# Optimization experiments

Measured on AMD Instinct MI355X. Metric: run time of the kernel, lower is better.

## Reference

```python
import jax, jax.numpy as jnp
import numpy as np


def setup_inputs() -> dict:
    key = jax.random.key(0)
    ks = jax.random.split(key, 7)
    B, S, D, KP = 16, 4096, 64, 256  # batch*heads, seq_len, head_dim, linformer proj dim
    Q = jax.random.normal(ks[0], (B, S, D), dtype=jnp.float32)
    K = jax.random.normal(ks[1], (B, S, D), dtype=jnp.float32)
    V = jax.random.normal(ks[2], (B, S, D), dtype=jnp.float32)
    E_w = jax.random.normal(ks[3], (KP, S), dtype=jnp.float32) / np.sqrt(S)
    E_b = jax.random.normal(ks[4], (KP,), dtype=jnp.float32) * 0.01
    F_w = jax.random.normal(ks[5], (KP, S), dtype=jnp.float32) / np.sqrt(S)
    F_b = jax.random.normal(ks[6], (KP,), dtype=jnp.float32) * 0.01
    return {"Q": Q, "K": K, "V": V, "E_w": E_w, "E_b": E_b, "F_w": F_w, "F_b": F_b}


def reference(Q, K, V, E_w, E_b, F_w, F_b):
    # Linformer head (mask=None path); dropout is identity at inference.
    dim_k = K.shape[-1]
    scale = 1.0 / jnp.sqrt(jnp.float32(dim_k))
    # K.permute(0,2,1) -> [B, d, S]; E projects seq axis S -> k: [B, d, k]
    Kp = jnp.einsum('bsd,ks->bdk', K, E_w) + E_b  # [B, d, k]
    # V.permute -> F -> permute back: [B, k, d]
    Vp = jnp.einsum('bsd,ks->bkd', V, F_w) + F_b[None, :, None]  # [B, k, d]
    scores = jnp.einsum('bsd,bdk->bsk', Q, Kp) * scale  # [B, S, k]
    attn = jax.nn.softmax(scores, axis=-1)
    out = jnp.einsum('bsk,bkd->bsd', attn, Vp)  # [B, S, d]
    return (out, attn)
```

## Files before the change

kernel.cpp:

```cpp
#include <hip/hip_runtime.h>


#define B_  16
#define S_  4096
#define D_  64
#define KP_ 256

typedef short v8s __attribute__((ext_vector_type(8)));
typedef float v4f __attribute__((ext_vector_type(4)));

__device__ __forceinline__ short f2bf(float x) {
    union { float f; unsigned u; } v; v.f = x;
    unsigned r = v.u + 0x7FFFu + ((v.u >> 16) & 1u);
    return (short)(r >> 16);
}
__device__ __forceinline__ float bf2f(short h) {
    union { float f; unsigned u; } v; v.u = ((unsigned)(unsigned short)h) << 16;
    return v.f;
}

__global__ __launch_bounds__(256)
void wcvt_kernel(const float* __restrict__ E_w, const float* __restrict__ F_w,
                 short* __restrict__ Whi, short* __restrict__ Wlo)
{
    const int p = blockIdx.y;
    const float* W = p ? F_w : E_w;
    const size_t i4 = (size_t)blockIdx.x * 256 + threadIdx.x;
    float4 v = ((const float4*)W)[i4];
    short4 h, lo;
    h.x = f2bf(v.x); lo.x = f2bf(v.x - bf2f(h.x));
    h.y = f2bf(v.y); lo.y = f2bf(v.y - bf2f(h.y));
    h.z = f2bf(v.z); lo.z = f2bf(v.z - bf2f(h.z));
    h.w = f2bf(v.w); lo.w = f2bf(v.w - bf2f(h.w));
    const int k  = (int)(i4 >> 10);
    const int s0 = (int)(i4 & 1023) << 2;
    const size_t fo = (((size_t)p * 16 + (k >> 4)) * 128 + (s0 >> 5)) * 512
                    + (size_t)(((k & 15) + ((s0 >> 3) & 3) * 16) * 8) + (s0 & 7);
    *(short4*)(Whi + fo) = h;
    *(short4*)(Wlo + fo) = lo;
}

__global__ __launch_bounds__(512, 4)
void proj_mfma_kernel(const float* __restrict__ Kg, const float* __restrict__ Vg,
                      const short* __restrict__ Whi, const short* __restrict__ Wlo,
                      float* __restrict__ PpartK, float* __restrict__ PpartV)
{
    const int sc = blockIdx.x;
    const int p  = blockIdx.y;
    const int b  = blockIdx.z;

    const float* src = (p ? Vg : Kg) + ((size_t)b * S_ + sc * 256) * D_;

    __shared__ __align__(16) short Af[2][2][4][512];

    const int t  = threadIdx.x;
    const int wv = t >> 6;
    const int l  = t & 63;
    const int k16 = wv * 2;

    const size_t wbase = (((size_t)p * 16 + k16) * 128 + sc * 8) * 512 + (size_t)l * 8;

    v4f acc[2][4];
#pragma unroll
    for (int i = 0; i < 2; ++i)
#pragma unroll
        for (int m = 0; m < 4; ++m) acc[i][m] = (v4f){0.f, 0.f, 0.f, 0.f};

    const bool do_stage = (t < 256);
    const int sd   = t & 63;
    const int soct = (t >> 6) & 3;
    const int smt  = sd >> 4;
    const int sfl  = (sd & 15) + soct * 16;

    float g[8];
    if (do_stage) {
        const float* sp = src + (size_t)(soct * 8) * D_ + sd;
#pragma unroll
        for (int j = 0; j < 8; ++j) g[j] = sp[(size_t)j * D_];
        v8s hi, lo;
#pragma unroll
        for (int j = 0; j < 8; ++j) { short h = f2bf(g[j]); hi[j] = h; lo[j] = f2bf(g[j] - bf2f(h)); }
        *(v8s*)&Af[0][0][smt][sfl * 8] = hi;
        *(v8s*)&Af[0][1][smt][sfl * 8] = lo;
    }
    __syncthreads();

    for (int st = 0; st < 8; ++st) {
        const int cur = st & 1;
        if (st + 1 < 8 && do_stage) {
            const float* sp = src + (size_t)((st + 1) * 32 + soct * 8) * D_ + sd;
#pragma unroll
            for (int j = 0; j < 8; ++j) g[j] = sp[(size_t)j * D_];
        }
        v8s wh[2], wl2[2];
#pragma unroll
        for (int i = 0; i < 2; ++i) {
            size_t o = wbase + (size_t)i * 65536 + (size_t)st * 512;
            wh[i]  = *(const v8s*)(Whi + o);
            wl2[i] = *(const v8s*)(Wlo + o);
        }
        v8s sh[4], sl[4];
#pragma unroll
        for (int m = 0; m < 4; ++m) {
            sh[m] = *(const v8s*)&Af[cur][0][m][l * 8];
            sl[m] = *(const v8s*)&Af[cur][1][m][l * 8];
        }
        if (p == 0) {
#pragma unroll
            for (int i = 0; i < 2; ++i)
#pragma unroll
                for (int m = 0; m < 4; ++m) {
                    acc[i][m] = __builtin_amdgcn_mfma_f32_16x16x32_bf16(wh[i],  sh[m], acc[i][m], 0, 0, 0);
                    acc[i][m] = __builtin_amdgcn_mfma_f32_16x16x32_bf16(wh[i],  sl[m], acc[i][m], 0, 0, 0);
                    acc[i][m] = __builtin_amdgcn_mfma_f32_16x16x32_bf16(wl2[i], sh[m], acc[i][m], 0, 0, 0);
                }
        } else {
#pragma unroll
            for (int i = 0; i < 2; ++i)
#pragma unroll
                for (int m = 0; m < 4; ++m) {
                    acc[i][m] = __builtin_amdgcn_mfma_f32_16x16x32_bf16(sh[m], wh[i],  acc[i][m], 0, 0, 0);
                    acc[i][m] = __builtin_amdgcn_mfma_f32_16x16x32_bf16(sl[m], wh[i],  acc[i][m], 0, 0, 0);
                    acc[i][m] = __builtin_amdgcn_mfma_f32_16x16x32_bf16(sh[m], wl2[i], acc[i][m], 0, 0, 0);
                }
        }
        if (st + 1 < 8 && do_stage) {
            v8s hi, lo;
#pragma unroll
            for (int j = 0; j < 8; ++j) { short h = f2bf(g[j]); hi[j] = h; lo[j] = f2bf(g[j] - bf2f(h)); }
            *(v8s*)&Af[cur ^ 1][0][smt][sfl * 8] = hi;
            *(v8s*)&Af[cur ^ 1][1][smt][sfl * 8] = lo;
        }
        __syncthreads();
    }

    const int krow0 = wv * 32;
    if (p == 0) {
        float* outp = PpartK + ((size_t)sc * B_ + b) * (KP_ * D_);
#pragma unroll
        for (int i = 0; i < 2; ++i)
#pragma unroll
            for (int m = 0; m < 4; ++m)
#pragma unroll
                for (int r = 0; r < 4; ++r) {
                    int k = krow0 + i * 16 + (l >> 4) * 4 + r;
                    int d = m * 16 + (l & 15);
                    outp[(size_t)k * D_ + d] = acc[i][m][r];
                }
    } else {
        float* outp = PpartV + ((size_t)sc * B_ + b) * (KP_ * D_);
#pragma unroll
        for (int i = 0; i < 2; ++i)
#pragma unroll
            for (int m = 0; m < 4; ++m)
#pragma unroll
                for (int r = 0; r < 4; ++r) {
                    int d = m * 16 + (l >> 4) * 4 + r;
                    int k = krow0 + i * 16 + (l & 15);
                    outp[(size_t)d * KP_ + k] = acc[i][m][r];
                }
    }
}

__global__ __launch_bounds__(256)
void reduce_kernel(const float* __restrict__ PpartK, const float* __restrict__ PpartV,
                   const float* __restrict__ E_b, const float* __restrict__ F_b,
                   short* __restrict__ Kp_hi, short* __restrict__ Kp_lo,
                   short* __restrict__ Vp_hi)
{
    const int j    = blockIdx.x * 256 + threadIdx.x;
    const int side = j >> 16;
    const int i4   = j & 65535;
    const int flat = i4 * 4;
    const int b    = flat >> 14;
    const int dk   = flat & 16383;

    if (side == 0) {
        float4 a = make_float4(0.f, 0.f, 0.f, 0.f);
#pragma unroll
        for (int sc = 0; sc < 16; ++sc) {
            float4 v = *(const float4*)(PpartK + ((size_t)sc * B_ + b) * (KP_ * D_) + dk);
            a.x += v.x; a.y += v.y; a.z += v.z; a.w += v.w;
        }
        const int k = dk >> 6, d = dk & 63;
        float be = E_b[k];
        a.x += be; a.y += be; a.z += be; a.w += be;
        short4 h, lo;
        h.x = f2bf(a.x); lo.x = f2bf(a.x - bf2f(h.x));
        h.y = f2bf(a.y); lo.y = f2bf(a.y - bf2f(h.y));
        h.z = f2bf(a.z); lo.z = f2bf(a.z - bf2f(h.z));
        h.w = f2bf(a.w); lo.w = f2bf(a.w - bf2f(h.w));
        const size_t fo = (((size_t)b * 2 + (d >> 5)) * 16 + (k >> 4)) * 512
                        + (size_t)((k & 15) + ((d >> 3) & 3) * 16) * 8 + (d & 7);
        *(short4*)(Kp_hi + fo) = h;
        *(short4*)(Kp_lo + fo) = lo;
    } else {
        float4 a = make_float4(0.f, 0.f, 0.f, 0.f);
#pragma unroll
        for (int sc = 0; sc < 16; ++sc) {
            float4 v = *(const float4*)(PpartV + ((size_t)sc * B_ + b) * (KP_ * D_) + dk);
            a.x += v.x; a.y += v.y; a.z += v.z; a.w += v.w;
        }
        const int d = dk >> 8, k = dk & 255;
        float4 bf = *(const float4*)(F_b + k);
        a.x += bf.x; a.y += bf.y; a.z += bf.z; a.w += bf.w;
        short4 h;
        h.x = f2bf(a.x); h.y = f2bf(a.y); h.z = f2bf(a.z); h.w = f2bf(a.w);
        const size_t fo = (((size_t)b * 8 + (k >> 5)) * 4 + (d >> 4)) * 512
                        + (size_t)((d & 15) + ((k >> 3) & 3) * 16) * 8 + (k & 7);
        *(short4*)(Vp_hi + fo) = h;
    }
}

__global__ __launch_bounds__(256, 3)
void attn_mfma_kernel(const float* __restrict__ Qg,
                      const short* __restrict__ Kp_hi, const short* __restrict__ Kp_lo,
                      const short* __restrict__ Vp_hi,
                      float* __restrict__ attn_out, float* __restrict__ outg)
{
    const int st = blockIdx.x;
    const int b  = blockIdx.y;
    const int t  = threadIdx.x;
    const int wv = t >> 6;
    const int l  = t & 63;

    __shared__ __align__(16) short smem[64 * 264];
    __shared__ __align__(16) float Fst[4][4][264];
    short (*Qf)[2][4][512] = (short (*)[2][4][512])smem;
    short* Pl  = smem;
    short* KLl = smem + 8192;
    short* KLh = (short*)&Fst[0][0][0];

    {
        const int s    = t & 63;
        const int doct = t >> 6;
        const float* qrow = Qg + ((size_t)b * S_ + st * 64 + s) * D_;
        const int mt = s >> 4, fl = (s & 15) + doct * 16;
#pragma unroll
        for (int kd = 0; kd < 2; ++kd) {
            float4 v0 = *(const float4*)(qrow + kd * 32 + doct * 8);
            float4 v1 = *(const float4*)(qrow + kd * 32 + doct * 8 + 4);
            float gq[8] = {v0.x, v0.y, v0.z, v0.w, v1.x, v1.y, v1.z, v1.w};
            v8s hi, lo;
#pragma unroll
            for (int jj = 0; jj < 8; ++jj) { short h = f2bf(gq[jj]); hi[jj] = h; lo[jj] = f2bf(gq[jj] - bf2f(h)); }
            *(v8s*)&Qf[kd][0][mt][fl * 8] = hi;
            *(v8s*)&Qf[kd][1][mt][fl * 8] = lo;
        }
    }
    __syncthreads();

    v4f acc2[16];
#pragma unroll
    for (int nt = 0; nt < 16; ++nt) acc2[nt] = (v4f){0.f, 0.f, 0.f, 0.f};
#pragma unroll
    for (int kd = 0; kd < 2; ++kd) {
        {
            const size_t tbl = (((size_t)b * 2 + kd) * 16) * 512;
            const int4* gh = (const int4*)(Kp_hi + tbl);
            const int4* gl = (const int4*)(Kp_lo + tbl);
            int4* lh = (int4*)KLh;
            int4* ll = (int4*)KLl;
#pragma unroll
            for (int i = 0; i < 4; ++i) lh[t + i * 256] = gh[t + i * 256];
#pragma unroll
            for (int i = 0; i < 4; ++i) ll[t + i * 256] = gl[t + i * 256];
        }
        __syncthreads();
        v8s Ah = *(const v8s*)&Qf[kd][0][wv][l * 8];
        v8s Al = *(const v8s*)&Qf[kd][1][wv][l * 8];
#pragma unroll
        for (int nt = 0; nt < 16; ++nt) {
            v8s Bh = *(const v8s*)&KLh[nt * 512 + l * 8];
            v8s Bl = *(const v8s*)&KLl[nt * 512 + l * 8];
            acc2[nt] = __builtin_amdgcn_mfma_f32_16x16x32_bf16(Ah, Bh, acc2[nt], 0, 0, 0);
            acc2[nt] = __builtin_amdgcn_mfma_f32_16x16x32_bf16(Al, Bh, acc2[nt], 0, 0, 0);
            acc2[nt] = __builtin_amdgcn_mfma_f32_16x16x32_bf16(Ah, Bl, acc2[nt], 0, 0, 0);
        }
        __syncthreads();
    }

    int4 vstg[4];
    {
        const int4* gv = (const int4*)(Vp_hi + (size_t)b * 16384);
#pragma unroll
        for (int i = 0; i < 4; ++i) vstg[i] = gv[t + i * 256];
    }

    const float scale = 0.125f;
    float* attn_b = attn_out + ((size_t)b * S_ + st * 64) * KP_;
    const int g = l >> 4;
#pragma unroll
    for (int r = 0; r < 4; ++r) {
        float m = -3.4e38f;
#pragma unroll
        for (int nt = 0; nt < 16; ++nt) m = fmaxf(m, acc2[nt][r]);
        m = fmaxf(m, __shfl_xor(m, 1));
        m = fmaxf(m, __shfl_xor(m, 2));
        m = fmaxf(m, __shfl_xor(m, 4));
        m = fmaxf(m, __shfl_xor(m, 8));
        float sum = 0.f;
#pragma unroll
        for (int nt = 0; nt < 16; ++nt) {
            float e = __expf((acc2[nt][r] - m) * scale);
            acc2[nt][r] = e; sum += e;
        }
        sum += __shfl_xor(sum, 1);
        sum += __shfl_xor(sum, 2);
        sum += __shfl_xor(sum, 4);
        sum += __shfl_xor(sum, 8);
        const float inv = 1.f / sum;
        const int s_loc = wv * 16 + g * 4 + r;
#pragma unroll
        for (int nt = 0; nt < 16; ++nt) {
            float pv = acc2[nt][r] * inv;
            Fst[wv][g][nt * 16 + (l & 15)] = pv;
            Pl[s_loc * 264 + nt * 16 + (l & 15)] = f2bf(pv);
        }
#pragma unroll
        for (int gg = 0; gg < 4; ++gg) {
            float4 vv = *(const float4*)&Fst[wv][gg][l * 4];
            *(float4*)(attn_b + (size_t)(wv * 16 + gg * 4 + r) * KP_ + l * 4) = vv;
        }
    }
    __syncthreads();
    {
        int4* lv = (int4*)KLh;
#pragma unroll
        for (int i = 0; i < 4; ++i) lv[t + i * 256] = vstg[i];
    }
    {
        const int4* gv2 = (const int4*)(Vp_hi + (size_t)b * 16384 + 8192);
#pragma unroll
        for (int i = 0; i < 4; ++i) vstg[i] = gv2[t + i * 256];
    }
    __syncthreads();
    v4f acc3[4];
#pragma unroll
    for (int nt = 0; nt < 4; ++nt) acc3[nt] = (v4f){0.f, 0.f, 0.f, 0.f};
#pragma unroll
    for (int kc = 0; kc < 4; ++kc) {
        v8s A3 = *(const v8s*)&Pl[(wv * 16 + (l & 15)) * 264 + kc * 32 + (l >> 4) * 8];
#pragma unroll
        for (int nt = 0; nt < 4; ++nt) {
            v8s B3 = *(const v8s*)&KLh[(kc * 4 + nt) * 512 + l * 8];
            acc3[nt] = __builtin_amdgcn_mfma_f32_16x16x32_bf16(A3, B3, acc3[nt], 0, 0, 0);
        }
    }
    __syncthreads();
    {
        int4* lv = (int4*)KLh;
#pragma unroll
        for (int i = 0; i < 4; ++i) lv[t + i * 256] = vstg[i];
    }
    __syncthreads();
#pragma unroll
    for (int kc = 4; kc < 8; ++kc) {
        v8s A3 = *(const v8s*)&Pl[(wv * 16 + (l & 15)) * 264 + kc * 32 + (l >> 4) * 8];
#pragma unroll
        for (int nt = 0; nt < 4; ++nt) {
            v8s B3 = *(const v8s*)&KLh[((kc - 4) * 4 + nt) * 512 + l * 8];
            acc3[nt] = __builtin_amdgcn_mfma_f32_16x16x32_bf16(A3, B3, acc3[nt], 0, 0, 0);
        }
    }
    float* out_b = outg + ((size_t)b * S_ + st * 64) * D_;
#pragma unroll
    for (int nt = 0; nt < 4; ++nt)
#pragma unroll
        for (int r = 0; r < 4; ++r) {
            int s_loc = wv * 16 + (l >> 4) * 4 + r;
            out_b[(size_t)s_loc * D_ + nt * 16 + (l & 15)] = acc3[nt][r];
        }
}

extern "C" void kernel_launch(void* const* d_in, const int* in_sizes, int n_in,
                              void* d_out, int out_size, void* d_ws, size_t ws_size,
                              hipStream_t stream) {
    const float* Q   = (const float*)d_in[0];
    const float* K   = (const float*)d_in[1];
    const float* V   = (const float*)d_in[2];
    const float* E_w = (const float*)d_in[3];
    const float* E_b = (const float*)d_in[4];
    const float* F_w = (const float*)d_in[5];
    const float* F_b = (const float*)d_in[6];

    float* out  = (float*)d_out;
    float* attn = out + (size_t)B_ * S_ * D_;

    short* Whi   = (short*)d_ws;
    short* Wlo   = Whi + (size_t)2 * KP_ * S_;
    short* Kp_hi = Wlo + (size_t)2 * KP_ * S_;
    short* Kp_lo = Kp_hi + (size_t)B_ * KP_ * D_;
    short* Vp_hi = Kp_lo + (size_t)B_ * KP_ * D_;

    float* PpartK = attn;
    float* PpartV = attn + (size_t)16 * B_ * KP_ * D_;

    wcvt_kernel<<<dim3(KP_ * S_ / 4 / 256, 2), 256, 0, stream>>>(E_w, F_w, Whi, Wlo);
    proj_mfma_kernel<<<dim3(16, 2, B_), 512, 0, stream>>>(K, V, Whi, Wlo, PpartK, PpartV);
    reduce_kernel<<<dim3(512), 256, 0, stream>>>(PpartK, PpartV, E_b, F_b, Kp_hi, Kp_lo, Vp_hi);
    attn_mfma_kernel<<<dim3(S_ / 64, B_), 256, 0, stream>>>(Q, Kp_hi, Kp_lo, Vp_hi, attn, out);
}
```

Measured before the change: 189.6 us.

## Process two batches per projection block to reuse weight fragments

Each projection block now handles two batch entries, with all 512 threads staging K/V data (256 per batch) into a doubled shared buffer. The weight hi/lo fragments loaded from global memory are reused across both batches, which halves weight traffic and doubles MFMA work per load. The cost is double the accumulator registers, which is why launch bounds drop to 2 blocks per SM, and the grid is halved to 256 blocks, lowering parallelism.

```diff
diff --git a/kernel.cpp b/kernel.cpp
--- a/kernel.cpp
+++ b/kernel.cpp
@@ -40,18 +40,18 @@
     *(short4*)(Wlo + fo) = lo;
 }
 
-__global__ __launch_bounds__(512, 4)
+__global__ __launch_bounds__(512, 2)
 void proj_mfma_kernel(const float* __restrict__ Kg, const float* __restrict__ Vg,
                       const short* __restrict__ Whi, const short* __restrict__ Wlo,
                       float* __restrict__ PpartK, float* __restrict__ PpartV)
 {
     const int sc = blockIdx.x;
     const int p  = blockIdx.y;
-    const int b  = blockIdx.z;
-
-    const float* src = (p ? Vg : Kg) + ((size_t)b * S_ + sc * 256) * D_;
-
-    __shared__ __align__(16) short Af[2][2][4][512];
+    const int bp = blockIdx.z;
+
+    const float* srcB = (p ? Vg : Kg);
+
+    __shared__ __align__(16) short Af[2][2][2][4][512];
 
     const int t  = threadIdx.x;
     const int wv = t >> 6;
@@ -60,35 +60,39 @@
 
     const size_t wbase = (((size_t)p * 16 + k16) * 128 + sc * 8) * 512 + (size_t)l * 8;
 
-    v4f acc[2][4];
-#pragma unroll
-    for (int i = 0; i < 2; ++i)
-#pragma unroll
-        for (int m = 0; m < 4; ++m) acc[i][m] = (v4f){0.f, 0.f, 0.f, 0.f};
-
-    const bool do_stage = (t < 256);
-    const int sd   = t & 63;
-    const int soct = (t >> 6) & 3;
+    v4f acc[2][2][4];
+#pragma unroll
+    for (int q = 0; q < 2; ++q)
+#pragma unroll
+        for (int i = 0; i < 2; ++i)
+#pragma unroll
+            for (int m = 0; m < 4; ++m) acc[q][i][m] = (v4f){0.f, 0.f, 0.f, 0.f};
+
+    const int bh   = t >> 8;
+    const int u    = t & 255;
+    const int sd   = u & 63;
+    const int soct = (u >> 6) & 3;
     const int smt  = sd >> 4;
     const int sfl  = (sd & 15) + soct * 16;
+    const float* mysrc = srcB + ((size_t)(bp * 2 + bh) * S_ + sc * 256) * D_;
 
     float g[8];
-    if (do_stage) {
-        const float* sp = src + (size_t)(soct * 8) * D_ + sd;
+    {
+        const float* sp = mysrc + (size_t)(soct * 8) * D_ + sd;
 #pragma unroll
         for (int j = 0; j < 8; ++j) g[j] = sp[(size_t)j * D_];
         v8s hi, lo;
 #pragma unroll
         for (int j = 0; j < 8; ++j) { short h = f2bf(g[j]); hi[j] = h; lo[j] = f2bf(g[j] - bf2f(h)); }
-        *(v8s*)&Af[0][0][smt][sfl * 8] = hi;
-        *(v8s*)&Af[0][1][smt][sfl * 8] = lo;
+        *(v8s*)&Af[0][bh][0][smt][sfl * 8] = hi;
+        *(v8s*)&Af[0][bh][1][smt][sfl * 8] = lo;
     }
     __syncthreads();
 
     for (int st = 0; st < 8; ++st) {
         const int cur = st & 1;
-        if (st + 1 < 8 && do_stage) {
-            const float* sp = src + (size_t)((st + 1) * 32 + soct * 8) * D_ + sd;
+        if (st + 1 < 8) {
+            const float* sp = mysrc + (size_t)((st + 1) * 32 + soct * 8) * D_ + sd;
 #pragma unroll
             for (int j = 0; j < 8; ++j) g[j] = sp[(size_t)j * D_];
         }
@@ -99,66 +103,73 @@
             wh[i]  = *(const v8s*)(Whi + o);
             wl2[i] = *(const v8s*)(Wlo + o);
         }
-        v8s sh[4], sl[4];
-#pragma unroll
-        for (int m = 0; m < 4; ++m) {
-            sh[m] = *(const v8s*)&Af[cur][0][m][l * 8];
-            sl[m] = *(const v8s*)&Af[cur][1][m][l * 8];
-        }
+#pragma unroll
+        for (int q = 0; q < 2; ++q) {
+            v8s sh[4], sl[4];
+#pragma unroll
+            for (int m = 0; m < 4; ++m) {
+                sh[m] = *(const v8s*)&Af[cur][q][0][m][l * 8];
+                sl[m] = *(const v8s*)&Af[cur][q][1][m][l * 8];
+            }
+            if (p == 0) {
+#pragma unroll
+                for (int i = 0; i < 2; ++i)
+#pragma unroll
+                    for (int m = 0; m < 4; ++m) {
+                        acc[q][i][m] = __builtin_amdgcn_mfma_f32_16x16x32_bf16(wh[i],  sh[m], acc[q][i][m], 0, 0, 0);
+                        acc[q][i][m] = __builtin_amdgcn_mfma_f32_16x16x32_bf16(wh[i],  sl[m], acc[q][i][m], 0, 0, 0);
+                        acc[q][i][m] = __builtin_amdgcn_mfma_f32_16x16x32_bf16(wl2[i], sh[m], acc[q][i][m], 0, 0, 0);
+                    }
+            } else {
+#pragma unroll
+                for (int i = 0; i < 2; ++i)
+#pragma unroll
+                    for (int m = 0; m < 4; ++m) {
+                        acc[q][i][m] = __builtin_amdgcn_mfma_f32_16x16x32_bf16(sh[m], wh[i],  acc[q][i][m], 0, 0, 0);
+                        acc[q][i][m] = __builtin_amdgcn_mfma_f32_16x16x32_bf16(sl[m], wh[i],  acc[q][i][m], 0, 0, 0);
+                        acc[q][i][m] = __builtin_amdgcn_mfma_f32_16x16x32_bf16(sh[m], wl2[i], acc[q][i][m], 0, 0, 0);
+                    }
+            }
+        }
+        if (st + 1 < 8) {
+            v8s hi, lo;
+#pragma unroll
+            for (int j = 0; j < 8; ++j) { short h = f2bf(g[j]); hi[j] = h; lo[j] = f2bf(g[j] - bf2f(h)); }
+            *(v8s*)&Af[cur ^ 1][bh][0][smt][sfl * 8] = hi;
+            *(v8s*)&Af[cur ^ 1][bh][1][smt][sfl * 8] = lo;
+        }
+        __syncthreads();
+    }
+
+    const int krow0 = wv * 32;
+#pragma unroll
+    for (int q = 0; q < 2; ++q) {
+        const int b = bp * 2 + q;
         if (p == 0) {
+            float* outp = PpartK + ((size_t)sc * B_ + b) * (KP_ * D_);
 #pragma unroll
             for (int i = 0; i < 2; ++i)
 #pragma unroll
-                for (int m = 0; m < 4; ++m) {
-                    acc[i][m] = __builtin_amdgcn_mfma_f32_16x16x32_bf16(wh[i],  sh[m], acc[i][m], 0, 0, 0);
-                    acc[i][m] = __builtin_amdgcn_mfma_f32_16x16x32_bf16(wh[i],  sl[m], acc[i][m], 0, 0, 0);
-                    acc[i][m] = __builtin_amdgcn_mfma_f32_16x16x32_bf16(wl2[i], sh[m], acc[i][m], 0, 0, 0);
-                }
+                for (int m = 0; m < 4; ++m)
+#pragma unroll
+                    for (int r = 0; r < 4; ++r) {
+                        int k = krow0 + i * 16 + (l >> 4) * 4 + r;
+                        int d = m * 16 + (l & 15);
+                        outp[(size_t)k * D_ + d] = acc[q][i][m][r];
+                    }
         } else {
+            float* outp = PpartV + ((size_t)sc * B_ + b) * (KP_ * D_);
 #pragma unroll
             for (int i = 0; i < 2; ++i)
 #pragma unroll
-                for (int m = 0; m < 4; ++m) {
-                    acc[i][m] = __builtin_amdgcn_mfma_f32_16x16x32_bf16(sh[m], wh[i],  acc[i][m], 0, 0, 0);
-                    acc[i][m] = __builtin_amdgcn_mfma_f32_16x16x32_bf16(sl[m], wh[i],  acc[i][m], 0, 0, 0);
-                    acc[i][m] = __builtin_amdgcn_mfma_f32_16x16x32_bf16(sh[m], wl2[i], acc[i][m], 0, 0, 0);
-                }
-        }
-        if (st + 1 < 8 && do_stage) {
-            v8s hi, lo;
-#pragma unroll
-            for (int j = 0; j < 8; ++j) { short h = f2bf(g[j]); hi[j] = h; lo[j] = f2bf(g[j] - bf2f(h)); }
-            *(v8s*)&Af[cur ^ 1][0][smt][sfl * 8] = hi;
-            *(v8s*)&Af[cur ^ 1][1][smt][sfl * 8] = lo;
-        }
-        __syncthreads();
-    }
-
-    const int krow0 = wv * 32;
-    if (p == 0) {
-        float* outp = PpartK + ((size_t)sc * B_ + b) * (KP_ * D_);
-#pragma unroll
-        for (int i = 0; i < 2; ++i)
-#pragma unroll
-            for (int m = 0; m < 4; ++m)
-#pragma unroll
-                for (int r = 0; r < 4; ++r) {
-                    int k = krow0 + i * 16 + (l >> 4) * 4 + r;
-                    int d = m * 16 + (l & 15);
-                    outp[(size_t)k * D_ + d] = acc[i][m][r];
-                }
-    } else {
-        float* outp = PpartV + ((size_t)sc * B_ + b) * (KP_ * D_);
-#pragma unroll
-        for (int i = 0; i < 2; ++i)
-#pragma unroll
-            for (int m = 0; m < 4; ++m)
-#pragma unroll
-                for (int r = 0; r < 4; ++r) {
-                    int d = m * 16 + (l >> 4) * 4 + r;
-                    int k = krow0 + i * 16 + (l & 15);
-                    outp[(size_t)d * KP_ + k] = acc[i][m][r];
-                }
+                for (int m = 0; m < 4; ++m)
+#pragma unroll
+                    for (int r = 0; r < 4; ++r) {
+                        int d = m * 16 + (l >> 4) * 4 + r;
+                        int k = krow0 + i * 16 + (l & 15);
+                        outp[(size_t)d * KP_ + k] = acc[q][i][m][r];
+                    }
+        }
     }
 }
 
@@ -397,7 +408,7 @@
     float* PpartV = attn + (size_t)16 * B_ * KP_ * D_;
 
     wcvt_kernel<<<dim3(KP_ * S_ / 4 / 256, 2), 256, 0, stream>>>(E_w, F_w, Whi, Wlo);
-    proj_mfma_kernel<<<dim3(16, 2, B_), 512, 0, stream>>>(K, V, Whi, Wlo, PpartK, PpartV);
+    proj_mfma_kernel<<<dim3(16, 2, 8), 512, 0, stream>>>(K, V, Whi, Wlo, PpartK, PpartV);
     reduce_kernel<<<dim3(512), 256, 0, stream>>>(PpartK, PpartV, E_b, F_b, Kp_hi, Kp_lo, Vp_hi);
     attn_mfma_kernel<<<dim3(S_ / 64, B_), 256, 0, stream>>>(Q, Kp_hi, Kp_lo, Vp_hi, attn, out);
 }
```

After: 189.5 us. No clear change (-0.1%).
